# Kernel tuning notes

Hardware: AMD Instinct MI355X
Metric: run time of the kernel (lower is better)

The kernel has to match this reference:

```python
import jax, jax.numpy as jnp
import numpy as np
from math import sqrt

BS, SEQ, NV, DM, K = 16, 1024, 512, 256, 8
EPS = 0.05  # sinkhorn epsilon
TEMP = 0.07  # concrete-bernoulli temperature


def setup_inputs() -> dict:
    key = jax.random.key(0)
    k1, k2, k3 = jax.random.split(key, 3)
    x = jax.random.normal(k1, (BS, SEQ, NV), jnp.float32)
    # nn.Linear(seq_len, d_model): weight [d_model, seq_len], bias [d_model]
    W = jax.random.normal(k2, (DM, SEQ), jnp.float32) / sqrt(SEQ)
    b = jnp.zeros((DM,), jnp.float32)
    cluster_emb = jax.random.normal(k3, (K, DM), jnp.float32) / sqrt(DM)
    return {"x": x, "W": W, "b": b, "cluster_emb": cluster_emb}


def _l2norm(z):
    # F.normalize(x, dim=1, p=2) with eps=1e-12 clamp
    n = jnp.maximum(jnp.linalg.norm(z, axis=1, keepdims=True), 1e-12)
    return z / n


def _sinkhorn(q):
    Q = jnp.exp(q / EPS)
    return Q / jnp.sum(Q, axis=1, keepdims=True)


def _concrete_bern(p, key):
    u = jax.random.uniform(key, p.shape, p.dtype, 1e-10, 1.0 - 1e-10)
    noise = jnp.log(u) - jnp.log1p(-u)
    logit = jnp.log(p + 1e-10) - jnp.log(1.0 - p + 1e-10)
    return jax.nn.sigmoid((logit + noise) / TEMP)


def _forward(x, W, b, cluster_emb):
    bs, S, nv = x.shape
    d = W.shape[0]
    k = cluster_emb.shape[0]
    # permute -> [bs, nv, S], Linear(S -> d)
    x_emb = jnp.einsum('bsv,ds->bvd', x, W) + b  # [bs, nv, d]
    x_flat = x_emb.reshape(-1, d)  # [bs*nv, d]
    # cosine-similarity cluster logits
    prob = (_l2norm(x_flat) @ _l2norm(cluster_emb).T).reshape(bs, nv, k)
    prob_temp = _sinkhorn(prob.reshape(-1, k)).reshape(bs, nv, k)  # individual probs
    prob_avg = _sinkhorn(jnp.mean(prob, axis=0))  # [nv, k]
    mask = _concrete_bern(prob_avg, jax.random.key(42))  # [nv, k]
    # CrossAttention with n_heads=1 (dropout inactive in eval)
    scale = 1.0 / sqrt(d)
    scores = jnp.einsum('kd,bvd->bkv', cluster_emb, x_emb)  # [bs, k, nv]
    A = jax.nn.softmax(scale * scores, axis=-1) * mask.T[None]  # masked attn
    V = jnp.einsum('bkv,bvd->bkd', A, x_emb)  # [bs, k, d]
    cluster_emb_avg = jnp.mean(V, axis=0)  # [k, d] (stored attribute in torch)
    # cluster_base_encoding: straight-through bernoulli, broadcast over seq_len
    soft = prob_temp.transpose(2, 0, 1)[..., None]  # [k, bs, nv, 1]
    u = jax.random.uniform(jax.random.key(7), soft.shape, soft.dtype)
    bern = (u < jax.lax.stop_gradient(soft)).astype(soft.dtype)
    extend = jnp.broadcast_to(bern, (k, bs, nv, S))  # [k, bs, nv, S]
    hard = soft + jax.lax.stop_gradient(extend - soft)  # straight-through
    return hard


def reference(x, W, b, cluster_emb):
    return _forward(x, W, b, cluster_emb)
```

## Files before the change

### kernel.cpp

```cpp
#include <hip/hip_runtime.h>
#include <hip/hip_bf16.h>
#include <math.h>
#include <stdint.h>

#define BS 16
#define SEQ 1024
#define NV 512
#define DM 256
#define NK 8

typedef float f32x2 __attribute__((ext_vector_type(2)));

__device__ double g_WC[NK * SEQ];
__device__ double g_Bk[NK];
__device__ __align__(16) float g_Wt[SEQ * DM];
__device__ __align__(16) float g_zp[4 * BS * NV * DM];
__device__ double g_nn2[BS * NV];
__device__ double g_Dp[8 * BS * NV * NK];
__device__ unsigned char g_bits[BS * NV];

__device__ __forceinline__ void threefry2x32_key7(uint32_t x0, uint32_t x1,
                                                  uint32_t& o0, uint32_t& o1) {
    const uint32_t k0 = 0u, k1 = 7u;
    const uint32_t k2 = k0 ^ k1 ^ 0x1BD11BDAu;
    uint32_t v0 = x0 + k0, v1 = x1 + k1;
#define TF_ROUND(r) { v0 += v1; v1 = (v1 << (r)) | (v1 >> (32 - (r))); v1 ^= v0; }
    TF_ROUND(13) TF_ROUND(15) TF_ROUND(26) TF_ROUND(6)
    v0 += k1; v1 += k2 + 1u;
    TF_ROUND(17) TF_ROUND(29) TF_ROUND(16) TF_ROUND(24)
    v0 += k2; v1 += k0 + 2u;
    TF_ROUND(13) TF_ROUND(15) TF_ROUND(26) TF_ROUND(6)
    v0 += k0; v1 += k1 + 3u;
    TF_ROUND(17) TF_ROUND(29) TF_ROUND(16) TF_ROUND(24)
    v0 += k1; v1 += k2 + 4u;
    TF_ROUND(13) TF_ROUND(15) TF_ROUND(26) TF_ROUND(6)
    v0 += k2; v1 += k0 + 5u;
#undef TF_ROUND
    o0 = v0; o1 = v1;
}

__device__ __forceinline__ float bits_to_uniform(uint32_t b) {
    return __uint_as_float((b >> 9) | 0x3F800000u) - 1.0f;
}

__global__ __launch_bounds__(256) void wtprep_kernel(
        const float* __restrict__ W, const float* __restrict__ bias,
        const float* __restrict__ ce) {
    __shared__ __align__(16) char smem[34816];
    const int t = threadIdx.x;

    if (blockIdx.x < 32) {
        double* red = (double*)smem;
        double* cen = (double*)(smem + 2048);
        const int k = blockIdx.x >> 2;
        const int schunk = blockIdx.x & 3;

        double c = (double)ce[k * DM + t];
        red[t] = c * c;
        __syncthreads();
        for (int off = 128; off > 0; off >>= 1) {
            if (t < off) red[t] += red[t + off];
            __syncthreads();
        }
        double nc = fmax(sqrt(red[0]), 1e-12);
        cen[t] = c / nc;
        __syncthreads();
        red[t] = (double)bias[t] * cen[t];
        __syncthreads();
        for (int off = 128; off > 0; off >>= 1) {
            if (t < off) red[t] += red[t + off];
            __syncthreads();
        }
        if (t == 0 && schunk == 0) g_Bk[k] = red[0];

        const int s = schunk * 256 + t;
        double acc = 0.0;
        for (int d = 0; d < DM; ++d)
            acc += cen[d] * (double)W[(size_t)d * SEQ + s];
        g_WC[(size_t)k * SEQ + s] = acc;
    } else {
        float* tile = (float*)smem;
        const int bx = blockIdx.x - 32;
        const int s0 = (bx & 15) * 64;
        const int d0 = (bx >> 4) * 128;
#pragma unroll
        for (int p = 0; p < 32; ++p) {
            int lin = p * 256 + t;
            int d = lin >> 6, s = lin & 63;
            tile[s * 132 + d] = W[(size_t)(d0 + d) * SEQ + s0 + s];
        }
        __syncthreads();
#pragma unroll
        for (int p = 0; p < 32; ++p) {
            int lin = p * 256 + t;
            int s = lin >> 7, d = lin & 127;
            g_Wt[(size_t)(s0 + s) * DM + d0 + d] = tile[s * 132 + d];
        }
    }
}

#define KC 32
#define XS_LD 132
#define WST_LD 320

__global__ __launch_bounds__(256, 1) void gemm_kernel(
        const float* __restrict__ x) {
    __shared__ __align__(16) float xs[KC * XS_LD];
    __shared__ __align__(16) float wst[KC * WST_LD];

    const int t = threadIdx.x;
    const int kblk = blockIdx.x;
    const int vblk = blockIdx.y;
    const int b    = blockIdx.z;
    const int v0 = vblk * 128;
    const float* xb = x + (size_t)b * SEQ * NV;

    const int tv8  = (t & 15) * 8;
    const int grp  = t >> 4;
    const int td16 = grp * 16;
    const int wofs = grp * 20;

    f32x2 acc[8][8];
#pragma unroll
    for (int j = 0; j < 8; ++j)
#pragma unroll
        for (int i = 0; i < 8; ++i) acc[j][i] = (f32x2){0.0f, 0.0f};

    const int sbeg = kblk * 256;
    for (int s0 = sbeg; s0 < sbeg + 256; s0 += KC) {
        __syncthreads();
#pragma unroll
        for (int j = 0; j < 4; ++j) {
            int lin = j * 256 + t;
            int sl = lin >> 5, c4 = (lin & 31) << 2;
            float4 val = *(const float4*)&xb[(size_t)(s0 + sl) * NV + v0 + c4];
            *(float4*)&xs[sl * XS_LD + c4] = val;
        }
#pragma unroll
        for (int j = 0; j < 8; ++j) {
            int lin = j * 256 + t;
            int sl = lin >> 6, c4 = (lin & 63) << 2;
            float4 val = *(const float4*)&g_Wt[(size_t)(s0 + sl) * DM + c4];
            *(float4*)&wst[sl * WST_LD + (c4 >> 4) * 20 + (c4 & 15)] = val;
        }
        __syncthreads();
#pragma unroll
        for (int kk = 0; kk < KC; ++kk) {
            const float* xr = &xs[kk * XS_LD + tv8];
            const float* wr = &wst[kk * WST_LD + wofs];
            float4 xv0 = *(const float4*)(xr);
            float4 xv1 = *(const float4*)(xr + 4);
            float4 wv0 = *(const float4*)(wr);
            float4 wv1 = *(const float4*)(wr + 4);
            float4 wv2 = *(const float4*)(wr + 8);
            float4 wv3 = *(const float4*)(wr + 12);
            float xv[8] = {xv0.x, xv0.y, xv0.z, xv0.w, xv1.x, xv1.y, xv1.z, xv1.w};
            f32x2 wp[8] = {{wv0.x, wv0.y}, {wv0.z, wv0.w},
                           {wv1.x, wv1.y}, {wv1.z, wv1.w},
                           {wv2.x, wv2.y}, {wv2.z, wv2.w},
                           {wv3.x, wv3.y}, {wv3.z, wv3.w}};
#pragma unroll
            for (int j = 0; j < 8; ++j) {
                f32x2 xd = {xv[j], xv[j]};
#pragma unroll
                for (int i = 0; i < 8; ++i)
                    asm("v_pk_fma_f32 %0, %1, %2, %0"
                        : "+v"(acc[j][i]) : "v"(xd), "v"(wp[i]));
            }
        }
    }

#pragma unroll
    for (int j = 0; j < 8; ++j) {
        size_t base = (size_t)kblk * (BS * NV * DM) +
                      ((size_t)b * NV + v0 + tv8 + j) * DM + td16;
#pragma unroll
        for (int m = 0; m < 4; ++m)
            *(float4*)&g_zp[base + 4 * m] =
                make_float4(acc[j][2 * m].x, acc[j][2 * m].y,
                            acc[j][2 * m + 1].x, acc[j][2 * m + 1].y);
    }
}

__global__ __launch_bounds__(256) void combine_kernel(
        const float* __restrict__ bias) {
    __shared__ double red[16][17];
    const int t = threadIdx.x;
    const int vg = blockIdx.x;
    const int b  = blockIdx.y;
    const int vl = t >> 4, dg = t & 15;
    const int v = vg * 16 + vl;

    const size_t bvbase = ((size_t)b * NV + v) * DM + dg * 16;
    double sq = 0.0;
#pragma unroll
    for (int m = 0; m < 16; m += 4) {
        float4 p0 = *(const float4*)&g_zp[(size_t)0 * (BS * NV * DM) + bvbase + m];
        float4 p1 = *(const float4*)&g_zp[(size_t)1 * (BS * NV * DM) + bvbase + m];
        float4 p2 = *(const float4*)&g_zp[(size_t)2 * (BS * NV * DM) + bvbase + m];
        float4 p3 = *(const float4*)&g_zp[(size_t)3 * (BS * NV * DM) + bvbase + m];
        float4 bb = *(const float4*)&bias[dg * 16 + m];
        double z0 = (double)p0.x + (double)p1.x + (double)p2.x + (double)p3.x + (double)bb.x;
        double z1 = (double)p0.y + (double)p1.y + (double)p2.y + (double)p3.y + (double)bb.y;
        double z2 = (double)p0.z + (double)p1.z + (double)p2.z + (double)p3.z + (double)bb.z;
        double z3 = (double)p0.w + (double)p1.w + (double)p2.w + (double)p3.w + (double)bb.w;
        sq += z0 * z0 + z1 * z1 + z2 * z2 + z3 * z3;
    }
    red[vl][dg] = sq;
    __syncthreads();
    if (dg == 0) {
        double s = 0.0;
#pragma unroll
        for (int i = 0; i < 16; ++i) s += red[vl][i];
        g_nn2[b * NV + v] = s;
    }
}

__global__ __launch_bounds__(256) void dkern(const float* __restrict__ x) {
    __shared__ double wcd[NK][128];
    __shared__ double dw[4][64][NK];
    const int t = threadIdx.x;
    const int vblk = blockIdx.x;
    const int b    = blockIdx.y;
    const int sc   = blockIdx.z;
    const int v0 = vblk * 64;
    const int ss = sc * 128;

#pragma unroll
    for (int j = 0; j < 4; ++j) {
        int idx = j * 256 + t;
        ((double*)wcd)[idx] = g_WC[(size_t)(idx >> 7) * SEQ + ss + (idx & 127)];
    }
    __syncthreads();

    const int vl = t & 63, w = t >> 6;
    const float* xp = x + (size_t)b * SEQ * NV + v0 + vl;
    double D[NK];
#pragma unroll
    for (int k = 0; k < NK; ++k) D[k] = 0.0;
    const int sw = w * 32;
    for (int i = 0; i < 32; ++i) {
        int sl = sw + i;
        double xv = (double)xp[(size_t)(ss + sl) * NV];
#pragma unroll
        for (int k = 0; k < NK; ++k) D[k] += xv * wcd[k][sl];
    }
#pragma unroll
    for (int k = 0; k < NK; ++k) dw[w][vl][k] = D[k];
    __syncthreads();

    const int v = t & 63, k2 = (t >> 6) * 2;
#pragma unroll
    for (int j = 0; j < 2; ++j) {
        int k = k2 + j;
        double s = dw[0][v][k] + dw[1][v][k] + dw[2][v][k] + dw[3][v][k];
        g_Dp[(((size_t)sc * BS + b) * NV + v0 + v) * NK + k] = s;
    }
}

__global__ __launch_bounds__(256) void finalize_kernel() {
    const int bv = blockIdx.x * 256 + threadIdx.x;
    double n = fmax(sqrt(g_nn2[bv]), 1e-12);

    double D[NK];
#pragma unroll
    for (int k = 0; k < NK; ++k) D[k] = g_Bk[k];
#pragma unroll
    for (int sc = 0; sc < 8; ++sc) {
#pragma unroll
        for (int k = 0; k < NK; ++k)
            D[k] += g_Dp[((size_t)sc * (BS * NV) + bv) * NK + k];
    }

    double p[NK], sum = 0.0;
#pragma unroll
    for (int k = 0; k < NK; ++k) {
        p[k] = exp((D[k] / n) / 0.05);
        sum += p[k];
    }
    unsigned int byte = 0;
#pragma unroll
    for (int k = 0; k < NK; ++k) {
        uint32_t i = (uint32_t)(k * (BS * NV) + bv);
        uint32_t y0, y1;
        threefry2x32_key7(0u, i, y0, y1);
        float u = bits_to_uniform(y0 ^ y1);
        if ((double)u < p[k] / sum) byte |= 1u << k;
    }
    g_bits[bv] = (unsigned char)byte;
}

__global__ __launch_bounds__(256) void write_kernel(float* __restrict__ out) {
    const int t = threadIdx.x;
    const size_t r0 = (size_t)blockIdx.x * 8;
#pragma unroll
    for (int j = 0; j < 8; ++j) {
        size_t r = r0 + j;
        unsigned int bv = (unsigned int)(r & 8191u);
        unsigned int k  = (unsigned int)(r >> 13);
        float v = ((g_bits[bv] >> k) & 1u) ? 1.0f : 0.0f;
        float4 val = make_float4(v, v, v, v);
        ((float4*)(out + r * 1024))[t] = val;
    }
}

extern "C" void kernel_launch(void* const* d_in, const int* in_sizes, int n_in,
                              void* d_out, int out_size, void* d_ws, size_t ws_size,
                              hipStream_t stream) {
    const float* x    = (const float*)d_in[0];
    const float* W    = (const float*)d_in[1];
    const float* bias = (const float*)d_in[2];
    const float* ce   = (const float*)d_in[3];
    float* out = (float*)d_out;

    wtprep_kernel<<<dim3(64), dim3(256), 0, stream>>>(W, bias, ce);
    gemm_kernel<<<dim3(4, 4, 16), dim3(256), 0, stream>>>(x);
    combine_kernel<<<dim3(32, 16), dim3(256), 0, stream>>>(bias);
    dkern<<<dim3(8, 16, 8), dim3(256), 0, stream>>>(x);
    finalize_kernel<<<dim3(32), dim3(256), 0, stream>>>();
    write_kernel<<<dim3(8192), dim3(256), 0, stream>>>(out);
}
```

Baseline: 394.1 us.

## Merge GEMM with dkern launch and fuse combine with finalize

After: 399.7 us. Within noise of the previous version (+1.4%).

```diff
diff --git a/kernel.cpp b/kernel.cpp
--- a/kernel.cpp
+++ b/kernel.cpp
@@ -9,13 +9,10 @@
 #define DM 256
 #define NK 8
 
-typedef float f32x2 __attribute__((ext_vector_type(2)));
-
 __device__ double g_WC[NK * SEQ];
 __device__ double g_Bk[NK];
 __device__ __align__(16) float g_Wt[SEQ * DM];
 __device__ __align__(16) float g_zp[4 * BS * NV * DM];
-__device__ double g_nn2[BS * NV];
 __device__ double g_Dp[8 * BS * NV * NK];
 __device__ unsigned char g_bits[BS * NV];
 
@@ -103,86 +100,131 @@
 #define XS_LD 132
 #define WST_LD 320
 
-__global__ __launch_bounds__(256, 1) void gemm_kernel(
+__global__ __launch_bounds__(256) void gemm_dkern_kernel(
         const float* __restrict__ x) {
-    __shared__ __align__(16) float xs[KC * XS_LD];
-    __shared__ __align__(16) float wst[KC * WST_LD];
+    __shared__ __align__(16) char smem[57856];
 
     const int t = threadIdx.x;
-    const int kblk = blockIdx.x;
-    const int vblk = blockIdx.y;
-    const int b    = blockIdx.z;
-    const int v0 = vblk * 128;
-    const float* xb = x + (size_t)b * SEQ * NV;
-
-    const int tv8  = (t & 15) * 8;
-    const int grp  = t >> 4;
-    const int td16 = grp * 16;
-    const int wofs = grp * 20;
-
-    f32x2 acc[8][8];
-#pragma unroll
-    for (int j = 0; j < 8; ++j)
-#pragma unroll
-        for (int i = 0; i < 8; ++i) acc[j][i] = (f32x2){0.0f, 0.0f};
-
-    const int sbeg = kblk * 256;
-    for (int s0 = sbeg; s0 < sbeg + 256; s0 += KC) {
-        __syncthreads();
+
+    if (blockIdx.x < 256) {
+        float* xs  = (float*)smem;
+        float* wst = (float*)(smem + 16896);
+
+        const int bx = blockIdx.x;
+        const int kblk = bx & 3;
+        const int vblk = (bx >> 2) & 3;
+        const int b    = bx >> 4;
+        const int v0 = vblk * 128;
+        const float* xb = x + (size_t)b * SEQ * NV;
+
+        const int tv8  = (t & 15) * 8;
+        const int grp  = t >> 4;
+        const int td16 = grp * 16;
+        const int wofs = grp * 20;
+
+        float acc[8][16];
+#pragma unroll
+        for (int j = 0; j < 8; ++j)
+#pragma unroll
+            for (int i = 0; i < 16; ++i) acc[j][i] = 0.0f;
+
+        const int sbeg = kblk * 256;
+        for (int s0 = sbeg; s0 < sbeg + 256; s0 += KC) {
+            __syncthreads();
+#pragma unroll
+            for (int j = 0; j < 4; ++j) {
+                int lin = j * 256 + t;
+                int sl = lin >> 5, c4 = (lin & 31) << 2;
+                float4 val = *(const float4*)&xb[(size_t)(s0 + sl) * NV + v0 + c4];
+                *(float4*)&xs[sl * XS_LD + c4] = val;
+            }
+#pragma unroll
+            for (int j = 0; j < 8; ++j) {
+                int lin = j * 256 + t;
+                int sl = lin >> 6, c4 = (lin & 63) << 2;
+                float4 val = *(const float4*)&g_Wt[(size_t)(s0 + sl) * DM + c4];
+                *(float4*)&wst[sl * WST_LD + (c4 >> 4) * 20 + (c4 & 15)] = val;
+            }
+            __syncthreads();
+#pragma unroll
+            for (int kk = 0; kk < KC; ++kk) {
+                const float* xr = &xs[kk * XS_LD + tv8];
+                const float* wr = &wst[kk * WST_LD + wofs];
+                float4 xv0 = *(const float4*)(xr);
+                float4 xv1 = *(const float4*)(xr + 4);
+                float4 wv0 = *(const float4*)(wr);
+                float4 wv1 = *(const float4*)(wr + 4);
+                float4 wv2 = *(const float4*)(wr + 8);
+                float4 wv3 = *(const float4*)(wr + 12);
+                float xv[8] = {xv0.x, xv0.y, xv0.z, xv0.w,
+                               xv1.x, xv1.y, xv1.z, xv1.w};
+                float wv[16] = {wv0.x, wv0.y, wv0.z, wv0.w,
+                                wv1.x, wv1.y, wv1.z, wv1.w,
+                                wv2.x, wv2.y, wv2.z, wv2.w,
+                                wv3.x, wv3.y, wv3.z, wv3.w};
+#pragma unroll
+                for (int j = 0; j < 8; ++j)
+#pragma unroll
+                    for (int i = 0; i < 16; ++i) acc[j][i] += xv[j] * wv[i];
+            }
+        }
+
+#pragma unroll
+        for (int j = 0; j < 8; ++j) {
+            size_t base = (size_t)kblk * (BS * NV * DM) +
+                          ((size_t)b * NV + v0 + tv8 + j) * DM + td16;
+#pragma unroll
+            for (int m = 0; m < 16; m += 4)
+                *(float4*)&g_zp[base + m] =
+                    make_float4(acc[j][m], acc[j][m + 1],
+                                acc[j][m + 2], acc[j][m + 3]);
+        }
+    } else {
+        double* wcd = (double*)smem;
+        double* dw  = (double*)(smem + 8192);
+
+        const int idx = blockIdx.x - 256;
+        const int vblk = idx & 7;
+        const int b    = (idx >> 3) & 15;
+        const int sc   = idx >> 7;
+        const int v0 = vblk * 64;
+        const int ss = sc * 128;
+
 #pragma unroll
         for (int j = 0; j < 4; ++j) {
-            int lin = j * 256 + t;
-            int sl = lin >> 5, c4 = (lin & 31) << 2;
-            float4 val = *(const float4*)&xb[(size_t)(s0 + sl) * NV + v0 + c4];
-            *(float4*)&xs[sl * XS_LD + c4] = val;
-        }
-#pragma unroll
-        for (int j = 0; j < 8; ++j) {
-            int lin = j * 256 + t;
-            int sl = lin >> 6, c4 = (lin & 63) << 2;
-            float4 val = *(const float4*)&g_Wt[(size_t)(s0 + sl) * DM + c4];
-            *(float4*)&wst[sl * WST_LD + (c4 >> 4) * 20 + (c4 & 15)] = val;
-        }
-        __syncthreads();
-#pragma unroll
-        for (int kk = 0; kk < KC; ++kk) {
-            const float* xr = &xs[kk * XS_LD + tv8];
-            const float* wr = &wst[kk * WST_LD + wofs];
-            float4 xv0 = *(const float4*)(xr);
-            float4 xv1 = *(const float4*)(xr + 4);
-            float4 wv0 = *(const float4*)(wr);
-            float4 wv1 = *(const float4*)(wr + 4);
-            float4 wv2 = *(const float4*)(wr + 8);
-            float4 wv3 = *(const float4*)(wr + 12);
-            float xv[8] = {xv0.x, xv0.y, xv0.z, xv0.w, xv1.x, xv1.y, xv1.z, xv1.w};
-            f32x2 wp[8] = {{wv0.x, wv0.y}, {wv0.z, wv0.w},
-                           {wv1.x, wv1.y}, {wv1.z, wv1.w},
-                           {wv2.x, wv2.y}, {wv2.z, wv2.w},
-                           {wv3.x, wv3.y}, {wv3.z, wv3.w}};
-#pragma unroll
-            for (int j = 0; j < 8; ++j) {
-                f32x2 xd = {xv[j], xv[j]};
-#pragma unroll
-                for (int i = 0; i < 8; ++i)
-                    asm("v_pk_fma_f32 %0, %1, %2, %0"
-                        : "+v"(acc[j][i]) : "v"(xd), "v"(wp[i]));
-            }
-        }
-    }
-
-#pragma unroll
-    for (int j = 0; j < 8; ++j) {
-        size_t base = (size_t)kblk * (BS * NV * DM) +
-                      ((size_t)b * NV + v0 + tv8 + j) * DM + td16;
-#pragma unroll
-        for (int m = 0; m < 4; ++m)
-            *(float4*)&g_zp[base + 4 * m] =
-                make_float4(acc[j][2 * m].x, acc[j][2 * m].y,
-                            acc[j][2 * m + 1].x, acc[j][2 * m + 1].y);
-    }
-}
-
-__global__ __launch_bounds__(256) void combine_kernel(
+            int i2 = j * 256 + t;
+            wcd[i2] = g_WC[(size_t)(i2 >> 7) * SEQ + ss + (i2 & 127)];
+        }
+        __syncthreads();
+
+        const int vl = t & 63, w = t >> 6;
+        const float* xp = x + (size_t)b * SEQ * NV + v0 + vl;
+        double D[NK];
+#pragma unroll
+        for (int k = 0; k < NK; ++k) D[k] = 0.0;
+        const int sw = w * 32;
+        for (int i = 0; i < 32; ++i) {
+            int sl = sw + i;
+            double xv = (double)xp[(size_t)(ss + sl) * NV];
+#pragma unroll
+            for (int k = 0; k < NK; ++k) D[k] += xv * wcd[k * 128 + sl];
+        }
+#pragma unroll
+        for (int k = 0; k < NK; ++k) dw[(w * 64 + vl) * NK + k] = D[k];
+        __syncthreads();
+
+        const int v = t & 63, k2 = (t >> 6) * 2;
+#pragma unroll
+        for (int j = 0; j < 2; ++j) {
+            int k = k2 + j;
+            double s = dw[(0 * 64 + v) * NK + k] + dw[(1 * 64 + v) * NK + k] +
+                       dw[(2 * 64 + v) * NK + k] + dw[(3 * 64 + v) * NK + k];
+            g_Dp[(((size_t)sc * BS + b) * NV + v0 + v) * NK + k] = s;
+        }
+    }
+}
+
+__global__ __launch_bounds__(256) void combine_fin_kernel(
         const float* __restrict__ bias) {
     __shared__ double red[16][17];
     const int t = threadIdx.x;
@@ -212,82 +254,37 @@
         double s = 0.0;
 #pragma unroll
         for (int i = 0; i < 16; ++i) s += red[vl][i];
-        g_nn2[b * NV + v] = s;
-    }
-}
-
-__global__ __launch_bounds__(256) void dkern(const float* __restrict__ x) {
-    __shared__ double wcd[NK][128];
-    __shared__ double dw[4][64][NK];
-    const int t = threadIdx.x;
-    const int vblk = blockIdx.x;
-    const int b    = blockIdx.y;
-    const int sc   = blockIdx.z;
-    const int v0 = vblk * 64;
-    const int ss = sc * 128;
-
-#pragma unroll
-    for (int j = 0; j < 4; ++j) {
-        int idx = j * 256 + t;
-        ((double*)wcd)[idx] = g_WC[(size_t)(idx >> 7) * SEQ + ss + (idx & 127)];
-    }
-    __syncthreads();
-
-    const int vl = t & 63, w = t >> 6;
-    const float* xp = x + (size_t)b * SEQ * NV + v0 + vl;
-    double D[NK];
-#pragma unroll
-    for (int k = 0; k < NK; ++k) D[k] = 0.0;
-    const int sw = w * 32;
-    for (int i = 0; i < 32; ++i) {
-        int sl = sw + i;
-        double xv = (double)xp[(size_t)(ss + sl) * NV];
-#pragma unroll
-        for (int k = 0; k < NK; ++k) D[k] += xv * wcd[k][sl];
-    }
-#pragma unroll
-    for (int k = 0; k < NK; ++k) dw[w][vl][k] = D[k];
-    __syncthreads();
-
-    const int v = t & 63, k2 = (t >> 6) * 2;
-#pragma unroll
-    for (int j = 0; j < 2; ++j) {
-        int k = k2 + j;
-        double s = dw[0][v][k] + dw[1][v][k] + dw[2][v][k] + dw[3][v][k];
-        g_Dp[(((size_t)sc * BS + b) * NV + v0 + v) * NK + k] = s;
-    }
-}
-
-__global__ __launch_bounds__(256) void finalize_kernel() {
-    const int bv = blockIdx.x * 256 + threadIdx.x;
-    double n = fmax(sqrt(g_nn2[bv]), 1e-12);
-
-    double D[NK];
-#pragma unroll
-    for (int k = 0; k < NK; ++k) D[k] = g_Bk[k];
-#pragma unroll
-    for (int sc = 0; sc < 8; ++sc) {
-#pragma unroll
-        for (int k = 0; k < NK; ++k)
-            D[k] += g_Dp[((size_t)sc * (BS * NV) + bv) * NK + k];
-    }
-
-    double p[NK], sum = 0.0;
-#pragma unroll
-    for (int k = 0; k < NK; ++k) {
-        p[k] = exp((D[k] / n) / 0.05);
-        sum += p[k];
-    }
-    unsigned int byte = 0;
-#pragma unroll
-    for (int k = 0; k < NK; ++k) {
-        uint32_t i = (uint32_t)(k * (BS * NV) + bv);
-        uint32_t y0, y1;
-        threefry2x32_key7(0u, i, y0, y1);
-        float u = bits_to_uniform(y0 ^ y1);
-        if ((double)u < p[k] / sum) byte |= 1u << k;
-    }
-    g_bits[bv] = (unsigned char)byte;
+
+        const int bv = b * NV + v;
+        double n = fmax(sqrt(s), 1e-12);
+
+        double D[NK];
+#pragma unroll
+        for (int k = 0; k < NK; ++k) D[k] = g_Bk[k];
+#pragma unroll
+        for (int sc = 0; sc < 8; ++sc) {
+#pragma unroll
+            for (int k = 0; k < NK; ++k)
+                D[k] += g_Dp[((size_t)sc * (BS * NV) + bv) * NK + k];
+        }
+
+        double p[NK], sum = 0.0;
+#pragma unroll
+        for (int k = 0; k < NK; ++k) {
+            p[k] = exp((D[k] / n) / 0.05);
+            sum += p[k];
+        }
+        unsigned int byte = 0;
+#pragma unroll
+        for (int k = 0; k < NK; ++k) {
+            uint32_t i = (uint32_t)(k * (BS * NV) + bv);
+            uint32_t y0, y1;
+            threefry2x32_key7(0u, i, y0, y1);
+            float u = bits_to_uniform(y0 ^ y1);
+            if ((double)u < p[k] / sum) byte |= 1u << k;
+        }
+        g_bits[bv] = (unsigned char)byte;
+    }
 }
 
 __global__ __launch_bounds__(256) void write_kernel(float* __restrict__ out) {
@@ -314,9 +311,7 @@
     float* out = (float*)d_out;
 
     wtprep_kernel<<<dim3(64), dim3(256), 0, stream>>>(W, bias, ce);
-    gemm_kernel<<<dim3(4, 4, 16), dim3(256), 0, stream>>>(x);
-    combine_kernel<<<dim3(32, 16), dim3(256), 0, stream>>>(bias);
-    dkern<<<dim3(8, 16, 8), dim3(256), 0, stream>>>(x);
-    finalize_kernel<<<dim3(32), dim3(256), 0, stream>>>();
+    gemm_dkern_kernel<<<dim3(1280), dim3(256), 0, stream>>>(x);
+    combine_fin_kernel<<<dim3(32, 16), dim3(256), 0, stream>>>(bias);
     write_kernel<<<dim3(8192), dim3(256), 0, stream>>>(out);
 }
```

## Fuse combine and finalize kernels; replace packed-FMA asm with scalar FMAs

Applied to the files above, without the earlier changes.

Measured after the change: 398.3 us. No clear change (+1.1%).

```diff
diff --git a/kernel.cpp b/kernel.cpp
--- a/kernel.cpp
+++ b/kernel.cpp
@@ -9,13 +9,10 @@
 #define DM 256
 #define NK 8
 
-typedef float f32x2 __attribute__((ext_vector_type(2)));
-
 __device__ double g_WC[NK * SEQ];
 __device__ double g_Bk[NK];
 __device__ __align__(16) float g_Wt[SEQ * DM];
 __device__ __align__(16) float g_zp[4 * BS * NV * DM];
-__device__ double g_nn2[BS * NV];
 __device__ double g_Dp[8 * BS * NV * NK];
 __device__ unsigned char g_bits[BS * NV];
 
@@ -120,11 +117,11 @@
     const int td16 = grp * 16;
     const int wofs = grp * 20;
 
-    f32x2 acc[8][8];
+    float acc[8][16];
 #pragma unroll
     for (int j = 0; j < 8; ++j)
 #pragma unroll
-        for (int i = 0; i < 8; ++i) acc[j][i] = (f32x2){0.0f, 0.0f};
+        for (int i = 0; i < 16; ++i) acc[j][i] = 0.0f;
 
     const int sbeg = kblk * 256;
     for (int s0 = sbeg; s0 < sbeg + 256; s0 += KC) {
@@ -155,18 +152,12 @@
             float4 wv2 = *(const float4*)(wr + 8);
             float4 wv3 = *(const float4*)(wr + 12);
             float xv[8] = {xv0.x, xv0.y, xv0.z, xv0.w, xv1.x, xv1.y, xv1.z, xv1.w};
-            f32x2 wp[8] = {{wv0.x, wv0.y}, {wv0.z, wv0.w},
-                           {wv1.x, wv1.y}, {wv1.z, wv1.w},
-                           {wv2.x, wv2.y}, {wv2.z, wv2.w},
-                           {wv3.x, wv3.y}, {wv3.z, wv3.w}};
-#pragma unroll
-            for (int j = 0; j < 8; ++j) {
-                f32x2 xd = {xv[j], xv[j]};
-#pragma unroll
-                for (int i = 0; i < 8; ++i)
-                    asm("v_pk_fma_f32 %0, %1, %2, %0"
-                        : "+v"(acc[j][i]) : "v"(xd), "v"(wp[i]));
-            }
+            float wv[16] = {wv0.x, wv0.y, wv0.z, wv0.w, wv1.x, wv1.y, wv1.z, wv1.w,
+                            wv2.x, wv2.y, wv2.z, wv2.w, wv3.x, wv3.y, wv3.z, wv3.w};
+#pragma unroll
+            for (int j = 0; j < 8; ++j)
+#pragma unroll
+                for (int i = 0; i < 16; ++i) acc[j][i] += xv[j] * wv[i];
         }
     }
 
@@ -175,14 +166,55 @@
         size_t base = (size_t)kblk * (BS * NV * DM) +
                       ((size_t)b * NV + v0 + tv8 + j) * DM + td16;
 #pragma unroll
-        for (int m = 0; m < 4; ++m)
-            *(float4*)&g_zp[base + 4 * m] =
-                make_float4(acc[j][2 * m].x, acc[j][2 * m].y,
-                            acc[j][2 * m + 1].x, acc[j][2 * m + 1].y);
-    }
-}
-
-__global__ __launch_bounds__(256) void combine_kernel(
+        for (int m = 0; m < 16; m += 4)
+            *(float4*)&g_zp[base + m] =
+                make_float4(acc[j][m], acc[j][m + 1], acc[j][m + 2], acc[j][m + 3]);
+    }
+}
+
+__global__ __launch_bounds__(256) void dkern(const float* __restrict__ x) {
+    __shared__ double wcd[NK][128];
+    __shared__ double dw[4][64][NK];
+    const int t = threadIdx.x;
+    const int vblk = blockIdx.x;
+    const int b    = blockIdx.y;
+    const int sc   = blockIdx.z;
+    const int v0 = vblk * 64;
+    const int ss = sc * 128;
+
+#pragma unroll
+    for (int j = 0; j < 4; ++j) {
+        int idx = j * 256 + t;
+        ((double*)wcd)[idx] = g_WC[(size_t)(idx >> 7) * SEQ + ss + (idx & 127)];
+    }
+    __syncthreads();
+
+    const int vl = t & 63, w = t >> 6;
+    const float* xp = x + (size_t)b * SEQ * NV + v0 + vl;
+    double D[NK];
+#pragma unroll
+    for (int k = 0; k < NK; ++k) D[k] = 0.0;
+    const int sw = w * 32;
+    for (int i = 0; i < 32; ++i) {
+        int sl = sw + i;
+        double xv = (double)xp[(size_t)(ss + sl) * NV];
+#pragma unroll
+        for (int k = 0; k < NK; ++k) D[k] += xv * wcd[k][sl];
+    }
+#pragma unroll
+    for (int k = 0; k < NK; ++k) dw[w][vl][k] = D[k];
+    __syncthreads();
+
+    const int v = t & 63, k2 = (t >> 6) * 2;
+#pragma unroll
+    for (int j = 0; j < 2; ++j) {
+        int k = k2 + j;
+        double s = dw[0][v][k] + dw[1][v][k] + dw[2][v][k] + dw[3][v][k];
+        g_Dp[(((size_t)sc * BS + b) * NV + v0 + v) * NK + k] = s;
+    }
+}
+
+__global__ __launch_bounds__(256) void combine_fin_kernel(
         const float* __restrict__ bias) {
     __shared__ double red[16][17];
     const int t = threadIdx.x;
@@ -212,82 +244,37 @@
         double s = 0.0;
 #pragma unroll
         for (int i = 0; i < 16; ++i) s += red[vl][i];
-        g_nn2[b * NV + v] = s;
-    }
-}
-
-__global__ __launch_bounds__(256) void dkern(const float* __restrict__ x) {
-    __shared__ double wcd[NK][128];
-    __shared__ double dw[4][64][NK];
-    const int t = threadIdx.x;
-    const int vblk = blockIdx.x;
-    const int b    = blockIdx.y;
-    const int sc   = blockIdx.z;
-    const int v0 = vblk * 64;
-    const int ss = sc * 128;
-
-#pragma unroll
-    for (int j = 0; j < 4; ++j) {
-        int idx = j * 256 + t;
-        ((double*)wcd)[idx] = g_WC[(size_t)(idx >> 7) * SEQ + ss + (idx & 127)];
-    }
-    __syncthreads();
-
-    const int vl = t & 63, w = t >> 6;
-    const float* xp = x + (size_t)b * SEQ * NV + v0 + vl;
-    double D[NK];
-#pragma unroll
-    for (int k = 0; k < NK; ++k) D[k] = 0.0;
-    const int sw = w * 32;
-    for (int i = 0; i < 32; ++i) {
-        int sl = sw + i;
-        double xv = (double)xp[(size_t)(ss + sl) * NV];
-#pragma unroll
-        for (int k = 0; k < NK; ++k) D[k] += xv * wcd[k][sl];
-    }
-#pragma unroll
-    for (int k = 0; k < NK; ++k) dw[w][vl][k] = D[k];
-    __syncthreads();
-
-    const int v = t & 63, k2 = (t >> 6) * 2;
-#pragma unroll
-    for (int j = 0; j < 2; ++j) {
-        int k = k2 + j;
-        double s = dw[0][v][k] + dw[1][v][k] + dw[2][v][k] + dw[3][v][k];
-        g_Dp[(((size_t)sc * BS + b) * NV + v0 + v) * NK + k] = s;
-    }
-}
-
-__global__ __launch_bounds__(256) void finalize_kernel() {
-    const int bv = blockIdx.x * 256 + threadIdx.x;
-    double n = fmax(sqrt(g_nn2[bv]), 1e-12);
-
-    double D[NK];
-#pragma unroll
-    for (int k = 0; k < NK; ++k) D[k] = g_Bk[k];
-#pragma unroll
-    for (int sc = 0; sc < 8; ++sc) {
-#pragma unroll
-        for (int k = 0; k < NK; ++k)
-            D[k] += g_Dp[((size_t)sc * (BS * NV) + bv) * NK + k];
-    }
-
-    double p[NK], sum = 0.0;
-#pragma unroll
-    for (int k = 0; k < NK; ++k) {
-        p[k] = exp((D[k] / n) / 0.05);
-        sum += p[k];
-    }
-    unsigned int byte = 0;
-#pragma unroll
-    for (int k = 0; k < NK; ++k) {
-        uint32_t i = (uint32_t)(k * (BS * NV) + bv);
-        uint32_t y0, y1;
-        threefry2x32_key7(0u, i, y0, y1);
-        float u = bits_to_uniform(y0 ^ y1);
-        if ((double)u < p[k] / sum) byte |= 1u << k;
-    }
-    g_bits[bv] = (unsigned char)byte;
+
+        const int bv = b * NV + v;
+        double n = fmax(sqrt(s), 1e-12);
+
+        double D[NK];
+#pragma unroll
+        for (int k = 0; k < NK; ++k) D[k] = g_Bk[k];
+#pragma unroll
+        for (int sc = 0; sc < 8; ++sc) {
+#pragma unroll
+            for (int k = 0; k < NK; ++k)
+                D[k] += g_Dp[((size_t)sc * (BS * NV) + bv) * NK + k];
+        }
+
+        double p[NK], sum = 0.0;
+#pragma unroll
+        for (int k = 0; k < NK; ++k) {
+            p[k] = exp((D[k] / n) / 0.05);
+            sum += p[k];
+        }
+        unsigned int byte = 0;
+#pragma unroll
+        for (int k = 0; k < NK; ++k) {
+            uint32_t i = (uint32_t)(k * (BS * NV) + bv);
+            uint32_t y0, y1;
+            threefry2x32_key7(0u, i, y0, y1);
+            float u = bits_to_uniform(y0 ^ y1);
+            if ((double)u < p[k] / sum) byte |= 1u << k;
+        }
+        g_bits[bv] = (unsigned char)byte;
+    }
 }
 
 __global__ __launch_bounds__(256) void write_kernel(float* __restrict__ out) {
@@ -315,8 +302,7 @@
 
     wtprep_kernel<<<dim3(64), dim3(256), 0, stream>>>(W, bias, ce);
     gemm_kernel<<<dim3(4, 4, 16), dim3(256), 0, stream>>>(x);
-    combine_kernel<<<dim3(32, 16), dim3(256), 0, stream>>>(bias);
     dkern<<<dim3(8, 16, 8), dim3(256), 0, stream>>>(x);
-    finalize_kernel<<<dim3(32), dim3(256), 0, stream>>>();
+    combine_fin_kernel<<<dim3(32, 16), dim3(256), 0, stream>>>(bias);
     write_kernel<<<dim3(8192), dim3(256), 0, stream>>>(out);
 }
```
